# Kernel optimization log

Hardware: AMD Instinct MI355X
Metric: run time of the kernel (lower is better)

Reference implementation:

```python
import jax, jax.numpy as jnp
import numpy as np
import math

L, D, H, PK, N = 3, 512, 8, 8, 3072
DK = D // H


def _layernorm(x, s, b):
    m = jnp.mean(x, axis=-1, keepdims=True)
    v = jnp.mean((x - m) ** 2, axis=-1, keepdims=True)
    return (x - m) / jnp.sqrt(v + 1e-6) * s + b


def setup_inputs() -> dict:
    key = jax.random.key(0)
    ks = jax.random.split(key, 12)
    p = lambda k, shape: jax.random.normal(k, shape, jnp.float32) * (1.0 / math.sqrt(shape[-1]))
    x = jax.random.normal(ks[0], (N, D), jnp.float32)
    adm = jax.random.randint(ks[1], (N, N), 0, PK, jnp.int32)
    return {
        "x": x,
        "adm": adm,
        "ln_att_s": jnp.ones((L, D), jnp.float32),
        "ln_att_b": jnp.zeros((L, D), jnp.float32),
        "Wq": p(ks[2], (L, D, D)),
        "Wk": p(ks[3], (L, D, D)),
        "Wv": p(ks[4], (L, D, D)),
        "rel_k": p(ks[5], (L, PK, DK)),
        "Wg": p(ks[6], (L, D, D)) * 0.0,  # gating weight init to 0 in original
        "bg": jnp.ones((L, D), jnp.float32),  # gating bias init to 1
        "Wo": p(ks[7], (L, D, D)),
        "bo": jnp.zeros((L, D), jnp.float32),
        "ln_ff_s": jnp.ones((L, D), jnp.float32),
        "ln_ff_b": jnp.zeros((L, D), jnp.float32),
        "W1": p(ks[8], (L, D, 2 * D)),
        "b1": jnp.zeros((L, 2 * D), jnp.float32),
        "W2": p(ks[9], (L, 2 * D, D)),
        "b2": jnp.zeros((L, D), jnp.float32),
    }


def reference(x, adm, ln_att_s, ln_att_b, Wq, Wk, Wv, rel_k, Wg, bg, Wo, bo,
              ln_ff_s, ln_ff_b, W1, b1, W2, b2):
    att_scores = []
    idx = jnp.broadcast_to(adm[None], (H, N, N))  # one_hot(gpm) @ r  ==  gather r along PK
    for n in range(L):
        xn = _layernorm(x, ln_att_s[n], ln_att_b[n])  # same layer_norm applied to x_q and x_k
        q = (xn @ Wq[n]).reshape(N, H, DK).transpose(1, 0, 2)  # [H,N,DK]
        k = (xn @ Wk[n]).reshape(N, H, DK).transpose(1, 0, 2)
        v = (xn @ Wv[n]).reshape(N, H, DK).transpose(1, 0, 2)
        attn1 = jnp.einsum('hid,hjd->hij', q, k)  # [H,N,N]
        rq = jnp.einsum('hid,pd->hip', q, rel_k[n])  # [H,N,PK]
        attn2 = jnp.take_along_axis(rq, idx, axis=2)  # [H,N,N]
        attn = jax.nn.softmax((attn1 + attn2) / math.sqrt(DK), axis=-1)
        out = jnp.einsum('hij,hjd->hid', attn, v).transpose(1, 0, 2).reshape(N, D)
        gate = jax.nn.sigmoid(xn @ Wg[n] + bg[n])
        m = (out * gate) @ Wo[n] + bo[n]
        # FFN with pre-layernorm, residual: x = x + pff(x + m)
        y = x + m
        yn = _layernorm(y, ln_ff_s[n], ln_ff_b[n])
        ff = jax.nn.gelu(yn @ W1[n] + b1[n], approximate=True) @ W2[n] + b2[n]
        x = x + ff
        att_scores.append(attn)
    return (x, jnp.stack(att_scores))
```

## Files before the change

kernel.cpp:

```cpp
#include <hip/hip_runtime.h>
#include <math.h>

#define NT 3072
#define DIM 512
#define NH 8
#define DKH 64
#define PKN 8
#define D2 1024
#define NL 3
#define QS 2048

typedef float4 f4;
typedef unsigned short ushort_t;
typedef unsigned char uchar_t;
typedef __attribute__((ext_vector_type(8))) short s8x;
typedef __attribute__((ext_vector_type(4))) float fx4;

#define MFMA(a, b, c) __builtin_amdgcn_mfma_f32_16x16x32_bf16(a, b, c, 0, 0, 0)
#define EX2(x) __builtin_amdgcn_exp2f(x)

__device__ __forceinline__ float b2f(ushort_t u) {
  union { unsigned int x; float f; } c;
  c.x = (unsigned int)u << 16;
  return c.f;
}
__device__ __forceinline__ ushort_t f2b(float f) {
  union { float f; unsigned int x; } c;
  c.f = f;
  unsigned int r = (c.x + 0x7FFFu + ((c.x >> 16) & 1u)) >> 16;
  return (ushort_t)r;
}
__device__ __forceinline__ float wred_sum(float v) {
#pragma unroll
  for (int off = 32; off > 0; off >>= 1) v += __shfl_xor(v, off);
  return v;
}
__device__ __forceinline__ void gload16(const ushort_t* g, ushort_t* l) {
  __builtin_amdgcn_global_load_lds(
      (const __attribute__((address_space(1))) unsigned int*)(const void*)g,
      (__attribute__((address_space(3))) unsigned int*)(void*)l, 16, 0, 0);
}

__global__ __launch_bounds__(256) void ln_bf16_kernel(
    const float* __restrict__ x, const float* __restrict__ s,
    const float* __restrict__ b, ushort_t* __restrict__ out) {
  int row = blockIdx.x;
  const float* xr = x + (size_t)row * DIM;
  int t = threadIdx.x;
  float v0 = xr[t], v1 = xr[t + 256];
  float sum = wred_sum(v0 + v1);
  float sq = wred_sum(v0 * v0 + v1 * v1);
  __shared__ float ss[4], s2[4];
  if ((t & 63) == 0) { ss[t >> 6] = sum; s2[t >> 6] = sq; }
  __syncthreads();
  float tot = ss[0] + ss[1] + ss[2] + ss[3];
  float tot2 = s2[0] + s2[1] + s2[2] + s2[3];
  float mean = tot * (1.0f / DIM);
  float var = tot2 * (1.0f / DIM) - mean * mean;
  float inv = rsqrtf(var + 1e-6f);
  ushort_t* orow = out + (size_t)row * DIM;
  orow[t] = f2b((v0 - mean) * inv * s[t] + b[t]);
  orow[t + 256] = f2b((v1 - mean) * inv * s[t + 256] + b[t + 256]);
}

__device__ __forceinline__ void tconv_body(const float* __restrict__ W,
                                           ushort_t* __restrict__ Wt, int K,
                                           int Nc, int tx, int ty) {
  __shared__ float Ls[64][65];
  int t = threadIdx.x;
  int n0 = tx * 64, k0 = ty * 64;
  int rr = t >> 4, cc = (t & 15) * 4;
#pragma unroll
  for (int p = 0; p < 4; ++p) {
    f4 v = *(const f4*)&W[(size_t)(k0 + rr + p * 16) * Nc + n0 + cc];
    Ls[rr + p * 16][cc + 0] = v.x;
    Ls[rr + p * 16][cc + 1] = v.y;
    Ls[rr + p * 16][cc + 2] = v.z;
    Ls[rr + p * 16][cc + 3] = v.w;
  }
  __syncthreads();
  int nr = t >> 2, kc = (t & 3) * 16;
  ushort_t tmp[16];
#pragma unroll
  for (int e = 0; e < 16; ++e) tmp[e] = f2b(Ls[kc + e][nr]);
  ushort_t* dst = &Wt[(size_t)(n0 + nr) * K + k0 + kc];
  *(uint4*)dst = *(uint4*)&tmp[0];
  *(uint4*)(dst + 8) = *(uint4*)&tmp[8];
}

__global__ __launch_bounds__(256) void wprep_kernel(
    const float* __restrict__ Wq, const float* __restrict__ Wk,
    const float* __restrict__ Wv, const float* __restrict__ Wg,
    const float* __restrict__ Wo, const float* __restrict__ W1,
    const float* __restrict__ W2, ushort_t* __restrict__ Wt) {
  int bid = blockIdx.x;
  if (bid < 320) {
    int job = bid >> 6, tile = bid & 63;
    const float* src = job == 0 ? Wq : job == 1 ? Wk : job == 2 ? Wv
                       : job == 3 ? Wg : Wo;
    tconv_body(src, Wt + (size_t)job * 262144, 512, 512, tile & 7, tile >> 3);
  } else if (bid < 448) {
    int tile = bid - 320;
    tconv_body(W1, Wt + 1310720, 512, 1024, tile & 15, tile >> 4);
  } else {
    int tile = bid - 448;
    tconv_body(W2, Wt + 1835008, 1024, 512, tile & 7, tile >> 3);
  }
}

__global__ __launch_bounds__(256) void adm8_kernel(const int* __restrict__ adm,
                                                   uchar_t* __restrict__ out) {
  size_t i = ((size_t)blockIdx.x * 256 + threadIdx.x) * 4;
  int4 v = *(const int4*)&adm[i];
  unsigned int b = (unsigned)(v.x & 255) | ((unsigned)(v.y & 255) << 8) |
                   ((unsigned)(v.z & 255) << 16) | ((unsigned)(v.w & 255) << 24);
  *(unsigned int*)&out[i] = b;
}

__global__ __launch_bounds__(256) void vt_kernel(const ushort_t* __restrict__ v,
                                                 ushort_t* __restrict__ vbT) {
  int jt = blockIdx.x, h = blockIdx.y;
  __shared__ ushort_t L[64][72];
  int t = threadIdx.x;
  int r = t >> 2, c = (t & 3) * 16;
  const ushort_t* src = v + (size_t)(jt * 64 + r) * QS + h * 64 + c;
  *(uint4*)&L[r][c] = *(const uint4*)src;
  *(uint4*)&L[r][c + 8] = *(const uint4*)(src + 8);
  __syncthreads();
  int d = t >> 2, j0 = (t & 3) * 16;
  ushort_t tmp[16];
#pragma unroll
  for (int e = 0; e < 16; ++e) tmp[e] = L[j0 + e][d];
  ushort_t* dst = vbT + (size_t)(h * 64 + d) * NT + jt * 64 + j0;
  *(uint4*)dst = *(uint4*)&tmp[0];
  *(uint4*)(dst + 8) = *(uint4*)&tmp[8];
}

template <int ACT, bool OBF>
__global__ __launch_bounds__(256) void gemm_bf16(
    const ushort_t* __restrict__ A, const ushort_t* __restrict__ mul, int ldm,
    const ushort_t* __restrict__ Bt, const float* __restrict__ bias,
    const float* __restrict__ res, void* __restrict__ Cp, int K, int ldc,
    float scale) {
  __shared__ __align__(16) ushort_t As[2048];
  __shared__ __align__(16) ushort_t Bs[2048];
  int t = threadIdx.x;
  int i0 = blockIdx.y * 64, j0 = blockIdx.x * 64;
  int w = t >> 6, l = t & 63;
  int wm = w >> 1, wn = w & 1;
  int lr = l >> 4, lc = l & 15;
  int fo = lr * 16 + (lc ^ (lr << 2));
  int am = t >> 2, akg = t & 3;
  int aoff = ((am >> 4) * 4 + akg) * 16 + ((am & 15) ^ (akg << 2));
  const ushort_t* Aptr = A + (size_t)(i0 + am) * K + akg * 8;
  const ushort_t* Mptr = mul ? mul + (size_t)(i0 + am) * ldm + akg * 8 : nullptr;
  int bc = l, bkg = w;
  int boff = ((bc >> 4) * 4 + bkg) * 16 + ((bc & 15) ^ (bkg << 2));
  const ushort_t* Bptr = Bt + (size_t)(j0 + bc) * K + bkg * 8;

  fx4 acc[2][2] = {};
  for (int k0 = 0; k0 < K; k0 += 32) {
    uint4 a = *(const uint4*)(Aptr + k0);
    if (mul) {
      uint4 m = *(const uint4*)(Mptr + k0);
      ushort_t* ap = (ushort_t*)&a;
      const ushort_t* mp = (const ushort_t*)&m;
#pragma unroll
      for (int e = 0; e < 8; ++e) ap[e] = f2b(b2f(ap[e]) * b2f(mp[e]));
    }
    *(uint4*)&As[aoff * 8] = a;
    *(uint4*)&Bs[boff * 8] = *(const uint4*)(Bptr + k0);
    __syncthreads();
    s8x a0 = *(const s8x*)&As[((wm * 2 + 0) * 64 + fo) * 8];
    s8x a1 = *(const s8x*)&As[((wm * 2 + 1) * 64 + fo) * 8];
    s8x b0 = *(const s8x*)&Bs[((wn * 2 + 0) * 64 + fo) * 8];
    s8x b1 = *(const s8x*)&Bs[((wn * 2 + 1) * 64 + fo) * 8];
    acc[0][0] = MFMA(a0, b0, acc[0][0]);
    acc[0][1] = MFMA(a0, b1, acc[0][1]);
    acc[1][0] = MFMA(a1, b0, acc[1][0]);
    acc[1][1] = MFMA(a1, b1, acc[1][1]);
    __syncthreads();
  }
#pragma unroll
  for (int ms = 0; ms < 2; ++ms) {
#pragma unroll
    for (int ns = 0; ns < 2; ++ns) {
#pragma unroll
      for (int r = 0; r < 4; ++r) {
        int i = i0 + (wm * 2 + ms) * 16 + lr * 4 + r;
        int j = j0 + (wn * 2 + ns) * 16 + lc;
        float o = acc[ms][ns][r] * scale;
        if (ACT == 3) {
          if (blockIdx.x < 8) o *= 0.18033688011112042f;
          if (blockIdx.x >= 24) {
            o += bias[j & 511];
            o = 1.0f / (1.0f + __expf(-o));
          }
        } else {
          if (bias) o += bias[j];
          if (ACT == 1) {
            o = 1.0f / (1.0f + __expf(-o));
          } else if (ACT == 2) {
            float xx = o;
            float c = 0.7978845608028654f * (xx + 0.044715f * xx * xx * xx);
            o = 0.5f * xx * (1.0f + tanhf(c));
          }
          if (res) o += res[(size_t)i * ldc + j];
        }
        if (OBF)
          ((ushort_t*)Cp)[(size_t)i * ldc + j] = f2b(o);
        else
          ((float*)Cp)[(size_t)i * ldc + j] = o;
      }
    }
  }
}

__device__ __forceinline__ float rq_sel(const unsigned int* rqt,
                                        unsigned int idx) {
  unsigned int d01 = (idx & 2) ? rqt[1] : rqt[0];
  unsigned int d23 = (idx & 2) ? rqt[3] : rqt[2];
  unsigned int dd = (idx & 4) ? d23 : d01;
  unsigned int r = (idx & 1) ? (dd & 0xffff0000u) : (dd << 16);
  return __uint_as_float(r);
}

__global__ __launch_bounds__(256) void attn_kernel(
    const ushort_t* __restrict__ xqkvg, const ushort_t* __restrict__ vbT,
    const float* __restrict__ relk, const uchar_t* __restrict__ adm8,
    float* __restrict__ att, ushort_t* __restrict__ av) {
  int h = blockIdx.y;
  int i0 = blockIdx.x * 32;
  int t = threadIdx.x, w = t >> 6, l = t & 63;
  int lr = l >> 4, lc = l & 15;
  int ig = w & 1, jh = w >> 1;
  int i_loc = ig * 16 + lc;
  int i = i0 + i_loc;

  __shared__ __align__(16) ushort_t Ks[2][4096];
  __shared__ __align__(16) ushort_t Vs[2][4096];
  __shared__ __align__(16) ushort_t Ps[2][2048];
  __shared__ float Od[32][68];
  __shared__ float MLs[2][2][16][2];

  const ushort_t* qp = xqkvg + (size_t)i * QS + h * 64 + lr * 8;
  s8x qf0 = *(const s8x*)qp;
  s8x qf1 = *(const s8x*)(qp + 32);

  unsigned int rqt[4];
  {
    const ushort_t* q0 = (const ushort_t*)&qf0;
    const ushort_t* q1 = (const ushort_t*)&qf1;
    float sp[8];
#pragma unroll
    for (int p = 0; p < 8; ++p) {
      const float* rp = relk + p * 64 + lr * 8;
      float s = 0.f;
#pragma unroll
      for (int e = 0; e < 8; ++e) s = fmaf(b2f(q0[e]), rp[e], s);
#pragma unroll
      for (int e = 0; e < 8; ++e) s = fmaf(b2f(q1[e]), rp[32 + e], s);
      s += __shfl_xor(s, 16);
      s += __shfl_xor(s, 32);
      sp[p] = s;
    }
#pragma unroll
    for (int j = 0; j < 4; ++j)
      rqt[j] = (unsigned int)f2b(sp[2 * j]) |
               ((unsigned int)f2b(sp[2 * j + 1]) << 16);
  }

  int stgo = (w & 1) * 2048;
  int srow = (w & 1) * 32 + (l >> 3);
  int kp8 = ((l & 7) ^ (l >> 3)) * 8;
  ushort_t* KS = Ks[jh];
  ushort_t* VS = Vs[jh];
  ushort_t* PS = Ps[jh];
  const ushort_t* kSrc0 =
      xqkvg + 512 + (size_t)(jh * 64 + srow) * QS + h * 64 + kp8;
  const ushort_t* vSrc0 = vbT + (size_t)(h * 64 + srow) * NT + jh * 64 + kp8;
  const uchar_t* admp0 = adm8 + (size_t)i * NT + jh * 64 + lr * 4;

  int sw = (lc & 7);
  int a_b0 = lc * 64 + ((lr ^ sw) << 3);
  int a_b1 = lc * 64 + (((4 + lr) ^ sw) << 3);
  int pb0 = i_loc * 64 + ((lr ^ sw) << 3);
  int pb1 = i_loc * 64 + (((4 + lr) ^ sw) << 3);
  int swz8 = sw << 3;

  float m_run = -1e30f, l_run = 0.f;

  {
    const ushort_t* kSrc = kSrc0;
    const uchar_t* admp = admp0;
    for (int tt = 0; tt < 24; ++tt) {
#pragma unroll
      for (int q = 0; q < 4; ++q)
        gload16(kSrc + (size_t)q * 8 * QS, KS + stgo + q * 512);
      __syncthreads();
      fx4 sacc[4] = {};
#pragma unroll
      for (int ja = 0; ja < 4; ++ja) {
        s8x a0 = *(const s8x*)(KS + a_b0 + ja * 1024);
        s8x a1 = *(const s8x*)(KS + a_b1 + ja * 1024);
        sacc[ja] = MFMA(a0, qf0, sacc[ja]);
        sacc[ja] = MFMA(a1, qf1, sacc[ja]);
      }
      float sv[4][4];
      float tm = -1e30f;
#pragma unroll
      for (int ja = 0; ja < 4; ++ja) {
        unsigned int aw = *(const unsigned int*)(admp + ja * 16);
#pragma unroll
        for (int r = 0; r < 4; ++r) {
          float vv = sacc[ja][r] + rq_sel(rqt, (aw >> (8 * r)) & 7u);
          sv[ja][r] = vv;
          tm = fmaxf(tm, vv);
        }
      }
      float mn = fmaxf(m_run, tm);
      float sum = 0.f;
#pragma unroll
      for (int ja = 0; ja < 4; ++ja)
#pragma unroll
        for (int r = 0; r < 4; ++r) sum += EX2(sv[ja][r] - mn);
      l_run = l_run * EX2(m_run - mn) + sum;
      m_run = mn;
      kSrc += (size_t)128 * QS;
      admp += 128;
      __syncthreads();
    }
  }
#pragma unroll
  for (int off = 16; off <= 32; off <<= 1) {
    float mo = __shfl_xor(m_run, off), lo = __shfl_xor(l_run, off);
    float mn = fmaxf(m_run, mo);
    l_run = l_run * EX2(m_run - mn) + lo * EX2(mo - mn);
    m_run = mn;
  }
  if (l < 16) {
    MLs[jh][ig][lc][0] = m_run;
    MLs[jh][ig][lc][1] = l_run;
  }
  __syncthreads();
  {
    float mo = MLs[jh ^ 1][ig][lc][0], lo = MLs[jh ^ 1][ig][lc][1];
    float mn = fmaxf(m_run, mo);
    l_run = l_run * EX2(m_run - mn) + lo * EX2(mo - mn);
    m_run = mn;
  }
  float lofs = m_run + __log2f(l_run);
  __syncthreads();

  fx4 oacc[4] = {};
  float* attb = att + ((size_t)h * NT + i0) * NT;
  int jh64 = jh * 64;
  {
    const ushort_t* kSrc = kSrc0;
    const ushort_t* vSrc = vSrc0;
    const uchar_t* admp = admp0;
    for (int tt = 0; tt < 24; ++tt) {
#pragma unroll
      for (int q = 0; q < 4; ++q) {
        gload16(kSrc + (size_t)q * 8 * QS, KS + stgo + q * 512);
        gload16(vSrc + (size_t)q * 8 * NT, VS + stgo + q * 512);
      }
      __syncthreads();
      fx4 sacc[4] = {};
#pragma unroll
      for (int ja = 0; ja < 4; ++ja) {
        s8x a0 = *(const s8x*)(KS + a_b0 + ja * 1024);
        s8x a1 = *(const s8x*)(KS + a_b1 + ja * 1024);
        sacc[ja] = MFMA(a0, qf0, sacc[ja]);
        sacc[ja] = MFMA(a1, qf1, sacc[ja]);
      }
#pragma unroll
      for (int ja = 0; ja < 4; ++ja) {
        unsigned int aw = *(const unsigned int*)(admp + ja * 16);
        float p0 = EX2(sacc[ja][0] + rq_sel(rqt, aw & 7u) - lofs);
        float p1 = EX2(sacc[ja][1] + rq_sel(rqt, (aw >> 8) & 7u) - lofs);
        float p2 = EX2(sacc[ja][2] + rq_sel(rqt, (aw >> 16) & 7u) - lofs);
        float p3 = EX2(sacc[ja][3] + rq_sel(rqt, (aw >> 24) & 7u) - lofs);
        unsigned int w01 =
            (unsigned int)f2b(p0) | ((unsigned int)f2b(p1) << 16);
        unsigned int w23 =
            (unsigned int)f2b(p2) | ((unsigned int)f2b(p3) << 16);
        int cb = ja * 16 + lr * 4;
        *(unsigned int*)&PS[i_loc * 64 + (cb ^ swz8)] = w01;
        *(unsigned int*)&PS[i_loc * 64 + ((cb + 2) ^ swz8)] = w23;
      }
      __syncthreads();
#pragma unroll
      for (int ks = 0; ks < 2; ++ks) {
        s8x pf = *(const s8x*)(PS + (ks == 0 ? pb0 : pb1));
#pragma unroll
        for (int nd = 0; nd < 4; ++nd) {
          s8x vf = *(const s8x*)(VS + (ks == 0 ? a_b0 : a_b1) + nd * 1024);
          oacc[nd] = MFMA(vf, pf, oacc[nd]);
        }
      }
      {
        int uu = (w & 1) * 64 + l;
        int row = uu >> 2, cs = (uu & 3) * 16;
        int rsw = (row & 7) << 3;
        uint4 A_ = *(const uint4*)&PS[row * 64 + (cs ^ rsw)];
        uint4 B_ = *(const uint4*)&PS[row * 64 + ((cs + 8) ^ rsw)];
        const ushort_t* ap = (const ushort_t*)&A_;
        const ushort_t* bp = (const ushort_t*)&B_;
        float* op = attb + (size_t)row * NT + tt * 128 + jh64 + cs;
        f4 o0 = {b2f(ap[0]), b2f(ap[1]), b2f(ap[2]), b2f(ap[3])};
        f4 o1 = {b2f(ap[4]), b2f(ap[5]), b2f(ap[6]), b2f(ap[7])};
        f4 o2 = {b2f(bp[0]), b2f(bp[1]), b2f(bp[2]), b2f(bp[3])};
        f4 o3 = {b2f(bp[4]), b2f(bp[5]), b2f(bp[6]), b2f(bp[7])};
        *(f4*)(op + 0) = o0;
        *(f4*)(op + 4) = o1;
        *(f4*)(op + 8) = o2;
        *(f4*)(op + 12) = o3;
      }
      kSrc += (size_t)128 * QS;
      vSrc += 128;
      admp += 128;
      __syncthreads();
    }
  }
  if (jh == 1) {
#pragma unroll
    for (int nd = 0; nd < 4; ++nd)
#pragma unroll
      for (int r = 0; r < 4; ++r) Od[i_loc][nd * 16 + lr * 4 + r] = oacc[nd][r];
  }
  __syncthreads();
  if (jh == 0) {
#pragma unroll
    for (int nd = 0; nd < 4; ++nd)
#pragma unroll
      for (int r = 0; r < 4; ++r)
        Od[i_loc][nd * 16 + lr * 4 + r] += oacc[nd][r];
  }
  __syncthreads();
  {
    int row = t >> 3, ds = (t & 7) * 8;
    f4 oA = *(const f4*)&Od[row][ds];
    f4 oB = *(const f4*)&Od[row][ds + 4];
    ushort_t tmp[8] = {f2b(oA.x), f2b(oA.y), f2b(oA.z), f2b(oA.w),
                       f2b(oB.x), f2b(oB.y), f2b(oB.z), f2b(oB.w)};
    *(uint4*)&av[(size_t)(i0 + row) * DIM + h * 64 + ds] = *(uint4*)tmp;
  }
}

extern "C" void kernel_launch(void* const* d_in, const int* in_sizes, int n_in,
                              void* d_out, int out_size, void* d_ws,
                              size_t ws_size, hipStream_t stream) {
  const float* x_in = (const float*)d_in[0];
  const int* adm = (const int*)d_in[1];
  const float* ln_att_s = (const float*)d_in[2];
  const float* ln_att_b = (const float*)d_in[3];
  const float* Wq = (const float*)d_in[4];
  const float* Wk = (const float*)d_in[5];
  const float* Wv = (const float*)d_in[6];
  const float* rel_k = (const float*)d_in[7];
  const float* Wg = (const float*)d_in[8];
  const float* bg = (const float*)d_in[9];
  const float* Wo = (const float*)d_in[10];
  const float* bo = (const float*)d_in[11];
  const float* ln_ff_s = (const float*)d_in[12];
  const float* ln_ff_b = (const float*)d_in[13];
  const float* W1 = (const float*)d_in[14];
  const float* b1 = (const float*)d_in[15];
  const float* W2 = (const float*)d_in[16];
  const float* b2 = (const float*)d_in[17];
  float* out = (float*)d_out;

  const size_t ND = (size_t)NT * DIM;
  char* ws = (char*)d_ws;
  float* x_cur = (float*)ws;
  float* y = (float*)(ws + 6291456);
  ushort_t* xqkvg = (ushort_t*)(ws + 12582912);
  ushort_t* avb = (ushort_t*)(ws + 25165824);
  ushort_t* xnb = (ushort_t*)(ws + 28311552);
  ushort_t* vbT = (ushort_t*)(ws + 31457280);
  uchar_t* adm8 = (uchar_t*)(ws + 34603008);
  ushort_t* Wt = (ushort_t*)(ws + 44040192);
  ushort_t* h1b = xqkvg;

  hipMemcpyAsync(x_cur, x_in, ND * sizeof(float), hipMemcpyDeviceToDevice,
                 stream);
  adm8_kernel<<<(NT * NT) / 1024, 256, 0, stream>>>(adm, adm8);

  dim3 gQKVG(32, NT / 64);
  dim3 gA(8, NT / 64);
  dim3 gF1(16, NT / 64);

  for (int n = 0; n < NL; ++n) {
    float* att = out + ND + (size_t)n * NH * NT * NT;
    size_t wo = (size_t)n * DIM * DIM;

    wprep_kernel<<<576, 256, 0, stream>>>(Wq + wo, Wk + wo, Wv + wo, Wg + wo,
                                          Wo + wo, W1 + (size_t)n * DIM * D2,
                                          W2 + (size_t)n * D2 * DIM, Wt);
    ln_bf16_kernel<<<NT, 256, 0, stream>>>(x_cur, ln_att_s + n * DIM,
                                           ln_att_b + n * DIM, xnb);
    gemm_bf16<3, true><<<gQKVG, 256, 0, stream>>>(
        xnb, nullptr, 0, Wt, bg + n * DIM, nullptr, xqkvg, DIM, QS, 1.0f);
    vt_kernel<<<dim3(NT / 64, NH), 256, 0, stream>>>(xqkvg + 1024, vbT);
    attn_kernel<<<dim3(NT / 32, NH), 256, 0, stream>>>(
        xqkvg, vbT, rel_k + n * PKN * DKH, adm8, att, avb);
    gemm_bf16<0, false><<<gA, 256, 0, stream>>>(
        avb, xqkvg + 1536, QS, Wt + 1048576, bo + n * DIM, x_cur, y, DIM, DIM,
        1.0f);
    ln_bf16_kernel<<<NT, 256, 0, stream>>>(y, ln_ff_s + n * DIM,
                                           ln_ff_b + n * DIM, xnb);
    gemm_bf16<2, true><<<gF1, 256, 0, stream>>>(xnb, nullptr, 0, Wt + 1310720,
                                                b1 + n * D2, nullptr, h1b, DIM,
                                                D2, 1.0f);
    gemm_bf16<0, false><<<gA, 256, 0, stream>>>(h1b, nullptr, 0, Wt + 1835008,
                                                b2 + n * DIM, x_cur, x_cur, D2,
                                                DIM, 1.0f);
  }
  hipMemcpyAsync(out, x_cur, ND * sizeof(float), hipMemcpyDeviceToDevice,
                 stream);
}
```

Before: 1.137 ms.

## Double-buffer GEMM and attention tile loads, fuse gating into attention epilogue

The GEMM now uses a K-step of 64 with double-buffered LDS tiles staged by async global-to-LDS loads, so the next tile loads while the current one is multiplied. The attention kernel likewise double-buffers its K and V tiles and remaps blocks so neighbouring blocks cover different heads. The gate multiply moves out of the Wo GEMM's A-load into the attention epilogue, and the two half-results are combined through bf16 LDS instead of a float buffer. GELU is rewritten with an exp-based sigmoid form. The extra buffers raise LDS use, which can reduce occupancy, and the bf16 intermediate in the combine step adds rounding.

```diff
diff --git a/kernel.cpp b/kernel.cpp
--- a/kernel.cpp
+++ b/kernel.cpp
@@ -137,58 +137,67 @@
 }
 
 template <int ACT, bool OBF>
-__global__ __launch_bounds__(256) void gemm_bf16(
-    const ushort_t* __restrict__ A, const ushort_t* __restrict__ mul, int ldm,
-    const ushort_t* __restrict__ Bt, const float* __restrict__ bias,
-    const float* __restrict__ res, void* __restrict__ Cp, int K, int ldc,
-    float scale) {
-  __shared__ __align__(16) ushort_t As[2048];
-  __shared__ __align__(16) ushort_t Bs[2048];
+__global__ __launch_bounds__(256) void gemm64(
+    const ushort_t* __restrict__ A, const ushort_t* __restrict__ Bt,
+    const float* __restrict__ bias, const float* __restrict__ res,
+    void* __restrict__ Cp, int K, int ldc, float scale) {
+  __shared__ __align__(16) ushort_t As[2][4096];
+  __shared__ __align__(16) ushort_t Bs[2][4096];
   int t = threadIdx.x;
   int i0 = blockIdx.y * 64, j0 = blockIdx.x * 64;
   int w = t >> 6, l = t & 63;
   int wm = w >> 1, wn = w & 1;
   int lr = l >> 4, lc = l & 15;
-  int fo = lr * 16 + (lc ^ (lr << 2));
-  int am = t >> 2, akg = t & 3;
-  int aoff = ((am >> 4) * 4 + akg) * 16 + ((am & 15) ^ (akg << 2));
-  const ushort_t* Aptr = A + (size_t)(i0 + am) * K + akg * 8;
-  const ushort_t* Mptr = mul ? mul + (size_t)(i0 + am) * ldm + akg * 8 : nullptr;
-  int bc = l, bkg = w;
-  int boff = ((bc >> 4) * 4 + bkg) * 16 + ((bc & 15) ^ (bkg << 2));
-  const ushort_t* Bptr = Bt + (size_t)(j0 + bc) * K + bkg * 8;
+  int sr = t >> 3;
+  int sc8 = ((t & 7) ^ (sr & 7)) * 8;
+  const ushort_t* aS = A + (size_t)(i0 + sr) * K + sc8;
+  const ushort_t* bS = Bt + (size_t)(j0 + sr) * K + sc8;
+  int sA0 = (wm * 32 + lc) * 64 + ((lr ^ (lc & 7)) * 8);
+  int sA1 = (wm * 32 + 16 + lc) * 64 + ((lr ^ (lc & 7)) * 8);
+  int sB0 = (wn * 32 + lc) * 64 + ((lr ^ (lc & 7)) * 8);
+  int sB1 = (wn * 32 + 16 + lc) * 64 + ((lr ^ (lc & 7)) * 8);
 
   fx4 acc[2][2] = {};
-  for (int k0 = 0; k0 < K; k0 += 32) {
-    uint4 a = *(const uint4*)(Aptr + k0);
-    if (mul) {
-      uint4 m = *(const uint4*)(Mptr + k0);
-      ushort_t* ap = (ushort_t*)&a;
-      const ushort_t* mp = (const ushort_t*)&m;
-#pragma unroll
-      for (int e = 0; e < 8; ++e) ap[e] = f2b(b2f(ap[e]) * b2f(mp[e]));
-    }
-    *(uint4*)&As[aoff * 8] = a;
-    *(uint4*)&Bs[boff * 8] = *(const uint4*)(Bptr + k0);
+
+#define G64_STAGE(buf, k0)                                                   \
+  {                                                                          \
+    gload16(aS + (k0), &As[buf][t * 8]);                                     \
+    gload16(aS + (k0) + (size_t)32 * K, &As[buf][2048 + t * 8]);             \
+    gload16(bS + (k0), &Bs[buf][t * 8]);                                     \
+    gload16(bS + (k0) + (size_t)32 * K, &Bs[buf][2048 + t * 8]);             \
+  }
+
+  G64_STAGE(0, 0);
+  __syncthreads();
+  int cur = 0;
+  for (int k0 = 0; k0 < K; k0 += 64) {
+    if (k0 + 64 < K) G64_STAGE(cur ^ 1, k0 + 64);
+    const ushort_t* Ac = As[cur];
+    const ushort_t* Bc = Bs[cur];
+#pragma unroll
+    for (int ks = 0; ks < 2; ++ks) {
+      s8x a0 = *(const s8x*)&Ac[sA0 ^ (ks << 5)];
+      s8x a1 = *(const s8x*)&Ac[sA1 ^ (ks << 5)];
+      s8x b0 = *(const s8x*)&Bc[sB0 ^ (ks << 5)];
+      s8x b1 = *(const s8x*)&Bc[sB1 ^ (ks << 5)];
+      acc[0][0] = MFMA(a0, b0, acc[0][0]);
+      acc[0][1] = MFMA(a0, b1, acc[0][1]);
+      acc[1][0] = MFMA(a1, b0, acc[1][0]);
+      acc[1][1] = MFMA(a1, b1, acc[1][1]);
+    }
     __syncthreads();
-    s8x a0 = *(const s8x*)&As[((wm * 2 + 0) * 64 + fo) * 8];
-    s8x a1 = *(const s8x*)&As[((wm * 2 + 1) * 64 + fo) * 8];
-    s8x b0 = *(const s8x*)&Bs[((wn * 2 + 0) * 64 + fo) * 8];
-    s8x b1 = *(const s8x*)&Bs[((wn * 2 + 1) * 64 + fo) * 8];
-    acc[0][0] = MFMA(a0, b0, acc[0][0]);
-    acc[0][1] = MFMA(a0, b1, acc[0][1]);
-    acc[1][0] = MFMA(a1, b0, acc[1][0]);
-    acc[1][1] = MFMA(a1, b1, acc[1][1]);
-    __syncthreads();
-  }
+    cur ^= 1;
+  }
+#undef G64_STAGE
+
 #pragma unroll
   for (int ms = 0; ms < 2; ++ms) {
 #pragma unroll
     for (int ns = 0; ns < 2; ++ns) {
 #pragma unroll
       for (int r = 0; r < 4; ++r) {
-        int i = i0 + (wm * 2 + ms) * 16 + lr * 4 + r;
-        int j = j0 + (wn * 2 + ns) * 16 + lc;
+        int i = i0 + wm * 32 + ms * 16 + lr * 4 + r;
+        int j = j0 + wn * 32 + ns * 16 + lc;
         float o = acc[ms][ns][r] * scale;
         if (ACT == 3) {
           if (blockIdx.x < 8) o *= 0.18033688011112042f;
@@ -202,8 +211,8 @@
             o = 1.0f / (1.0f + __expf(-o));
           } else if (ACT == 2) {
             float xx = o;
-            float c = 0.7978845608028654f * (xx + 0.044715f * xx * xx * xx);
-            o = 0.5f * xx * (1.0f + tanhf(c));
+            float c2 = 1.5957691216057308f * (xx + 0.044715f * xx * xx * xx);
+            o = xx / (1.0f + __expf(-c2));
           }
           if (res) o += res[(size_t)i * ldc + j];
         }
@@ -229,19 +238,46 @@
     const ushort_t* __restrict__ xqkvg, const ushort_t* __restrict__ vbT,
     const float* __restrict__ relk, const uchar_t* __restrict__ adm8,
     float* __restrict__ att, ushort_t* __restrict__ av) {
-  int h = blockIdx.y;
-  int i0 = blockIdx.x * 32;
+  int f = blockIdx.y * (NT / 32) + blockIdx.x;
+  int h = f & 7;
+  int i0 = (f >> 3) * 32;
   int t = threadIdx.x, w = t >> 6, l = t & 63;
   int lr = l >> 4, lc = l & 15;
   int ig = w & 1, jh = w >> 1;
   int i_loc = ig * 16 + lc;
   int i = i0 + i_loc;
 
-  __shared__ __align__(16) ushort_t Ks[2][4096];
-  __shared__ __align__(16) ushort_t Vs[2][4096];
+  __shared__ __align__(16) ushort_t Kd[2][2][4096];
+  __shared__ __align__(16) ushort_t Vd[2][2][4096];
   __shared__ __align__(16) ushort_t Ps[2][2048];
-  __shared__ float Od[32][68];
   __shared__ float MLs[2][2][16][2];
+
+  int stgo = ig * 2048;
+  int srow = ig * 32 + (l >> 3);
+  int kp8 = ((l & 7) ^ ((l >> 3) & 7)) * 8;
+  const ushort_t* kSrc0 =
+      xqkvg + 512 + (size_t)(jh * 64 + srow) * QS + h * 64 + kp8;
+  const ushort_t* vSrc0 = vbT + (size_t)(h * 64 + srow) * NT + jh * 64 + kp8;
+  const uchar_t* admp0 = adm8 + (size_t)i * NT + jh * 64 + lr * 4;
+
+#define STAGE_K(buf, tt)                                                     \
+  {                                                                          \
+    const ushort_t* ks_ = kSrc0 + (size_t)(tt) * 128 * QS;                   \
+    gload16(ks_, Kd[buf][jh] + stgo);                                        \
+    gload16(ks_ + (size_t)8 * QS, Kd[buf][jh] + stgo + 512);                 \
+    gload16(ks_ + (size_t)16 * QS, Kd[buf][jh] + stgo + 1024);               \
+    gload16(ks_ + (size_t)24 * QS, Kd[buf][jh] + stgo + 1536);               \
+  }
+#define STAGE_V(buf, tt)                                                     \
+  {                                                                          \
+    const ushort_t* vs_ = vSrc0 + (tt) * 128;                                \
+    gload16(vs_, Vd[buf][jh] + stgo);                                        \
+    gload16(vs_ + (size_t)8 * NT, Vd[buf][jh] + stgo + 512);                 \
+    gload16(vs_ + (size_t)16 * NT, Vd[buf][jh] + stgo + 1024);               \
+    gload16(vs_ + (size_t)24 * NT, Vd[buf][jh] + stgo + 1536);               \
+  }
+
+  STAGE_K(0, 0);
 
   const ushort_t* qp = xqkvg + (size_t)i * QS + h * 64 + lr * 8;
   s8x qf0 = *(const s8x*)qp;
@@ -269,17 +305,6 @@
       rqt[j] = (unsigned int)f2b(sp[2 * j]) |
                ((unsigned int)f2b(sp[2 * j + 1]) << 16);
   }
-
-  int stgo = (w & 1) * 2048;
-  int srow = (w & 1) * 32 + (l >> 3);
-  int kp8 = ((l & 7) ^ (l >> 3)) * 8;
-  ushort_t* KS = Ks[jh];
-  ushort_t* VS = Vs[jh];
-  ushort_t* PS = Ps[jh];
-  const ushort_t* kSrc0 =
-      xqkvg + 512 + (size_t)(jh * 64 + srow) * QS + h * 64 + kp8;
-  const ushort_t* vSrc0 = vbT + (size_t)(h * 64 + srow) * NT + jh * 64 + kp8;
-  const uchar_t* admp0 = adm8 + (size_t)i * NT + jh * 64 + lr * 4;
 
   int sw = (lc & 7);
   int a_b0 = lc * 64 + ((lr ^ sw) << 3);
@@ -289,15 +314,14 @@
   int swz8 = sw << 3;
 
   float m_run = -1e30f, l_run = 0.f;
+  __syncthreads();
 
   {
-    const ushort_t* kSrc = kSrc0;
-    const uchar_t* admp = admp0;
+    int cur = 0;
     for (int tt = 0; tt < 24; ++tt) {
-#pragma unroll
-      for (int q = 0; q < 4; ++q)
-        gload16(kSrc + (size_t)q * 8 * QS, KS + stgo + q * 512);
-      __syncthreads();
+      if (tt < 23) STAGE_K(cur ^ 1, tt + 1);
+      const ushort_t* KS = Kd[cur][jh];
+      const uchar_t* admp = admp0 + tt * 128;
       fx4 sacc[4] = {};
 #pragma unroll
       for (int ja = 0; ja < 4; ++ja) {
@@ -326,11 +350,14 @@
         for (int r = 0; r < 4; ++r) sum += EX2(sv[ja][r] - mn);
       l_run = l_run * EX2(m_run - mn) + sum;
       m_run = mn;
-      kSrc += (size_t)128 * QS;
-      admp += 128;
       __syncthreads();
-    }
-  }
+      cur ^= 1;
+    }
+  }
+
+  STAGE_K(0, 0);
+  STAGE_V(0, 0);
+
 #pragma unroll
   for (int off = 16; off <= 32; off <<= 1) {
     float mo = __shfl_xor(m_run, off), lo = __shfl_xor(l_run, off);
@@ -350,22 +377,21 @@
     m_run = mn;
   }
   float lofs = m_run + __log2f(l_run);
-  __syncthreads();
 
   fx4 oacc[4] = {};
   float* attb = att + ((size_t)h * NT + i0) * NT;
+  ushort_t* PS = Ps[jh];
   int jh64 = jh * 64;
   {
-    const ushort_t* kSrc = kSrc0;
-    const ushort_t* vSrc = vSrc0;
-    const uchar_t* admp = admp0;
+    int cur = 0;
     for (int tt = 0; tt < 24; ++tt) {
-#pragma unroll
-      for (int q = 0; q < 4; ++q) {
-        gload16(kSrc + (size_t)q * 8 * QS, KS + stgo + q * 512);
-        gload16(vSrc + (size_t)q * 8 * NT, VS + stgo + q * 512);
-      }
-      __syncthreads();
+      if (tt < 23) {
+        STAGE_K(cur ^ 1, tt + 1);
+        STAGE_V(cur ^ 1, tt + 1);
+      }
+      const ushort_t* KS = Kd[cur][jh];
+      const ushort_t* VS = Vd[cur][jh];
+      const uchar_t* admp = admp0 + tt * 128;
       fx4 sacc[4] = {};
 #pragma unroll
       for (int ja = 0; ja < 4; ++ja) {
@@ -381,26 +407,14 @@
         float p1 = EX2(sacc[ja][1] + rq_sel(rqt, (aw >> 8) & 7u) - lofs);
         float p2 = EX2(sacc[ja][2] + rq_sel(rqt, (aw >> 16) & 7u) - lofs);
         float p3 = EX2(sacc[ja][3] + rq_sel(rqt, (aw >> 24) & 7u) - lofs);
-        unsigned int w01 =
-            (unsigned int)f2b(p0) | ((unsigned int)f2b(p1) << 16);
-        unsigned int w23 =
-            (unsigned int)f2b(p2) | ((unsigned int)f2b(p3) << 16);
+        unsigned int w01 = (unsigned int)f2b(p0) | ((unsigned int)f2b(p1) << 16);
+        unsigned int w23 = (unsigned int)f2b(p2) | ((unsigned int)f2b(p3) << 16);
         int cb = ja * 16 + lr * 4;
         *(unsigned int*)&PS[i_loc * 64 + (cb ^ swz8)] = w01;
         *(unsigned int*)&PS[i_loc * 64 + ((cb + 2) ^ swz8)] = w23;
       }
-      __syncthreads();
-#pragma unroll
-      for (int ks = 0; ks < 2; ++ks) {
-        s8x pf = *(const s8x*)(PS + (ks == 0 ? pb0 : pb1));
-#pragma unroll
-        for (int nd = 0; nd < 4; ++nd) {
-          s8x vf = *(const s8x*)(VS + (ks == 0 ? a_b0 : a_b1) + nd * 1024);
-          oacc[nd] = MFMA(vf, pf, oacc[nd]);
-        }
-      }
       {
-        int uu = (w & 1) * 64 + l;
+        int uu = ig * 64 + l;
         int row = uu >> 2, cs = (uu & 3) * 16;
         int rsw = (row & 7) << 3;
         uint4 A_ = *(const uint4*)&PS[row * 64 + (cs ^ rsw)];
@@ -417,34 +431,52 @@
         *(f4*)(op + 8) = o2;
         *(f4*)(op + 12) = o3;
       }
-      kSrc += (size_t)128 * QS;
-      vSrc += 128;
-      admp += 128;
+#pragma unroll
+      for (int ks = 0; ks < 2; ++ks) {
+        s8x pf = *(const s8x*)(PS + (ks == 0 ? pb0 : pb1));
+#pragma unroll
+        for (int nd = 0; nd < 4; ++nd) {
+          s8x vf = *(const s8x*)(VS + (ks == 0 ? a_b0 : a_b1) + nd * 1024);
+          oacc[nd] = MFMA(vf, pf, oacc[nd]);
+        }
+      }
       __syncthreads();
-    }
-  }
+      cur ^= 1;
+    }
+  }
+#undef STAGE_K
+#undef STAGE_V
+
+  ushort_t* PsF = &Ps[0][0];
+  int swzO = (i_loc & 7) << 3;
   if (jh == 1) {
 #pragma unroll
-    for (int nd = 0; nd < 4; ++nd)
-#pragma unroll
-      for (int r = 0; r < 4; ++r) Od[i_loc][nd * 16 + lr * 4 + r] = oacc[nd][r];
+    for (int nd = 0; nd < 4; ++nd) {
+      int d0 = nd * 16 + lr * 4;
+      unsigned int lo = (unsigned int)f2b(oacc[nd][0]) |
+                        ((unsigned int)f2b(oacc[nd][1]) << 16);
+      unsigned int hi = (unsigned int)f2b(oacc[nd][2]) |
+                        ((unsigned int)f2b(oacc[nd][3]) << 16);
+      uint2 pk = {lo, hi};
+      *(uint2*)&PsF[i_loc * 64 + (d0 ^ swzO)] = pk;
+    }
   }
   __syncthreads();
   if (jh == 0) {
-#pragma unroll
-    for (int nd = 0; nd < 4; ++nd)
+    const ushort_t* gp = xqkvg + (size_t)i * QS + 1536 + h * 64;
+#pragma unroll
+    for (int nd = 0; nd < 4; ++nd) {
+      int d0 = nd * 16 + lr * 4;
+      uint2 pk = *(const uint2*)&PsF[i_loc * 64 + (d0 ^ swzO)];
+      const ushort_t* pp = (const ushort_t*)&pk;
+      uint2 gk = *(const uint2*)(gp + d0);
+      const ushort_t* gg = (const ushort_t*)&gk;
+      ushort_t ot[4];
 #pragma unroll
       for (int r = 0; r < 4; ++r)
-        Od[i_loc][nd * 16 + lr * 4 + r] += oacc[nd][r];
-  }
-  __syncthreads();
-  {
-    int row = t >> 3, ds = (t & 7) * 8;
-    f4 oA = *(const f4*)&Od[row][ds];
-    f4 oB = *(const f4*)&Od[row][ds + 4];
-    ushort_t tmp[8] = {f2b(oA.x), f2b(oA.y), f2b(oA.z), f2b(oA.w),
-                       f2b(oB.x), f2b(oB.y), f2b(oB.z), f2b(oB.w)};
-    *(uint4*)&av[(size_t)(i0 + row) * DIM + h * 64 + ds] = *(uint4*)tmp;
+        ot[r] = f2b((oacc[nd][r] + b2f(pp[r])) * b2f(gg[r]));
+      *(uint2*)&av[(size_t)i * DIM + h * 64 + d0] = *(uint2*)ot;
+    }
   }
 }
 
@@ -500,22 +532,19 @@
                                           W2 + (size_t)n * D2 * DIM, Wt);
     ln_bf16_kernel<<<NT, 256, 0, stream>>>(x_cur, ln_att_s + n * DIM,
                                            ln_att_b + n * DIM, xnb);
-    gemm_bf16<3, true><<<gQKVG, 256, 0, stream>>>(
-        xnb, nullptr, 0, Wt, bg + n * DIM, nullptr, xqkvg, DIM, QS, 1.0f);
+    gemm64<3, true><<<gQKVG, 256, 0, stream>>>(xnb, Wt, bg + n * DIM, nullptr,
+                                               xqkvg, DIM, QS, 1.0f);
     vt_kernel<<<dim3(NT / 64, NH), 256, 0, stream>>>(xqkvg + 1024, vbT);
     attn_kernel<<<dim3(NT / 32, NH), 256, 0, stream>>>(
         xqkvg, vbT, rel_k + n * PKN * DKH, adm8, att, avb);
-    gemm_bf16<0, false><<<gA, 256, 0, stream>>>(
-        avb, xqkvg + 1536, QS, Wt + 1048576, bo + n * DIM, x_cur, y, DIM, DIM,
-        1.0f);
+    gemm64<0, false><<<gA, 256, 0, stream>>>(avb, Wt + 1048576, bo + n * DIM,
+                                             x_cur, y, DIM, DIM, 1.0f);
     ln_bf16_kernel<<<NT, 256, 0, stream>>>(y, ln_ff_s + n * DIM,
                                            ln_ff_b + n * DIM, xnb);
-    gemm_bf16<2, true><<<gF1, 256, 0, stream>>>(xnb, nullptr, 0, Wt + 1310720,
-                                                b1 + n * D2, nullptr, h1b, DIM,
-                                                D2, 1.0f);
-    gemm_bf16<0, false><<<gA, 256, 0, stream>>>(h1b, nullptr, 0, Wt + 1835008,
-                                                b2 + n * DIM, x_cur, x_cur, D2,
-                                                DIM, 1.0f);
+    gemm64<2, true><<<gF1, 256, 0, stream>>>(xnb, Wt + 1310720, b1 + n * D2,
+                                             nullptr, h1b, DIM, D2, 1.0f);
+    gemm64<0, false><<<gA, 256, 0, stream>>>(h1b, Wt + 1835008, b2 + n * DIM,
+                                             x_cur, x_cur, D2, DIM, 1.0f);
   }
   hipMemcpyAsync(out, x_cur, ND * sizeof(float), hipMemcpyDeviceToDevice,
                  stream);
```

Measured after the change: 1.057 ms. 1.08x faster.
